# Optimization experiments

Measured on AMD Instinct MI355X. Metric: run time of the kernel, lower is better.

## Reference

```python
import jax, jax.numpy as jnp
import numpy as np

B, S, D = 2, 2048, 1024
H = 16
HD = D // H


def setup_inputs() -> dict:
    key = jax.random.key(0)
    ks = jax.random.split(key, 6)
    X = jax.random.normal(ks[0], (B, S, D), dtype=jnp.float32)
    # Linear weights stored [in, out] so y = x @ W (torch stores transposed).
    sc = 1.0 / np.sqrt(D)
    Wq = jax.random.normal(ks[1], (D, D), dtype=jnp.float32) * sc
    Wk = jax.random.normal(ks[2], (D, D), dtype=jnp.float32) * sc
    Wv = jax.random.normal(ks[3], (D, D), dtype=jnp.float32) * sc
    Wo = jax.random.normal(ks[4], (D, D), dtype=jnp.float32) * sc
    bo = jax.random.normal(ks[5], (D,), dtype=jnp.float32) * 0.01
    return {"X": X, "Wq": Wq, "Wk": Wk, "Wv": Wv, "Wo": Wo, "bo": bo}


def reference(X, Wq, Wk, Wv, Wo, bo):
    b, n, _ = X.shape
    # QKV projections (no bias, qkv_bias=False), reshape to [b, h, n, hd]
    q = (X @ Wq).reshape(b, n, H, HD).transpose(0, 2, 1, 3)
    k = (X @ Wk).reshape(b, n, H, HD).transpose(0, 2, 1, 3)
    v = (X @ Wv).reshape(b, n, H, HD).transpose(0, 2, 1, 3)
    # Unscaled scores (module's scale flag defaults to False)
    scores = jnp.einsum("bhqd,bhkd->bhqk", q, k)
    causal = jnp.triu(jnp.ones((n, n), dtype=bool), k=1)  # True above diagonal
    scores = jnp.where(causal, -jnp.inf, scores)
    attn = jax.nn.softmax(scores, axis=-1)
    # dropout p=0.0 -> identity
    ctx = jnp.einsum("bhqk,bhkd->bqhd", attn, v).reshape(b, n, H * HD)
    return ctx @ Wo + bo
```

## Files before the change

### kernel.cpp

```cpp
#include <hip/hip_runtime.h>
#include <stdint.h>


typedef __attribute__((ext_vector_type(8))) short short8;
typedef __attribute__((ext_vector_type(4))) float floatx4;

#define S_LEN 2048
#define D_DIM 1024
#define NH 16
#define HD 64
#define L2E 1.44269504088896340736f

__device__ __forceinline__ short f2bf(float f) {
    uint32_t u = __builtin_bit_cast(uint32_t, f);
    uint32_t r = u + 0x7fffu + ((u >> 16) & 1u);
    return (short)(r >> 16);
}
__device__ __forceinline__ uint32_t pack2(float a, float b) {
#if __has_builtin(__builtin_amdgcn_cvt_pk_bf16_f32)
    auto v = __builtin_amdgcn_cvt_pk_bf16_f32(a, b);
    uint32_t r; __builtin_memcpy(&r, &v, sizeof(r)); return r;
#else
    return (uint32_t)(uint16_t)f2bf(a) | ((uint32_t)(uint16_t)f2bf(b) << 16);
#endif
}
__device__ __forceinline__ void gll16(const void* g, void* l) {
    __builtin_amdgcn_global_load_lds(
        (const __attribute__((address_space(1))) void*)g,
        (__attribute__((address_space(3))) void*)l, 16, 0, 0);
}

__global__ __launch_bounds__(256) void castx_kernel(const float* __restrict__ X,
                                                    short* __restrict__ Xb) {
    int i = blockIdx.x * 256 + threadIdx.x;
    const float4 v = *(const float4*)(X + (size_t)i * 4);
    uint2 o;
    o.x = pack2(v.x, v.y);
    o.y = pack2(v.z, v.w);
    *(uint2*)(Xb + (size_t)i * 4) = o;
}

__global__ __launch_bounds__(256) void tcast4_kernel(const float* __restrict__ Wq,
                                                     const float* __restrict__ Wk,
                                                     const float* __restrict__ Wv,
                                                     const float* __restrict__ Wo,
                                                     short* __restrict__ WqkvT,
                                                     short* __restrict__ WoT) {
    const int z = blockIdx.z;
    const float* W = (z == 0) ? Wq : (z == 1) ? Wk : (z == 2) ? Wv : Wo;
    short* WT = (z < 3) ? (WqkvT + (size_t)z * 1024 * 1024) : WoT;
    __shared__ float tile[32][33];
    const int bx = blockIdx.x * 32;
    const int by = blockIdx.y * 32;
    const int tx = threadIdx.x, ty = threadIdx.y;
    for (int i = 0; i < 32; i += 8)
        tile[ty + i][tx] = W[(size_t)(bx + ty + i) * D_DIM + by + tx];
    __syncthreads();
    for (int i = 0; i < 32; i += 8)
        WT[(size_t)(by + ty + i) * D_DIM + bx + tx] = f2bf(tile[tx][ty + i]);
}

__device__ __forceinline__ void gemm_main8(const short* __restrict__ A,
                                           const short* __restrict__ BT,
                                           short* As, short* Bs,
                                           int m0, int n0, floatx4 (&acc)[4][2],
                                           int tid) {
    const int lane = tid & 63, ln = lane & 15, quad = lane >> 4;
    const int wave = tid >> 6;
    const int mw = (wave & 1) * 64, nw = (wave >> 1) * 32;
    for (int k0 = 0; k0 < D_DIM; k0 += 64) {
        __syncthreads();
        for (int t = 0; t < 2; t++) {
            const int c = t * 512 + tid;
            const int row = c >> 3, pos = c & 7, src = pos ^ (row & 7);
            gll16(A  + (size_t)(m0 + row) * D_DIM + k0 + src * 8, As + c * 8);
            gll16(BT + (size_t)(n0 + row) * D_DIM + k0 + src * 8, Bs + c * 8);
        }
        __syncthreads();
        for (int ks = 0; ks < 2; ks++) {
            short8 a[4], b[2];
            for (int i = 0; i < 4; i++) {
                const int row = mw + i * 16 + ln;
                a[i] = *(const short8*)(As + row * 64 + (((ks * 4 + quad) ^ (ln & 7)) * 8));
            }
            for (int j = 0; j < 2; j++) {
                const int row = nw + j * 16 + ln;
                b[j] = *(const short8*)(Bs + row * 64 + (((ks * 4 + quad) ^ (ln & 7)) * 8));
            }
            for (int i = 0; i < 4; i++)
                for (int j = 0; j < 2; j++)
                    acc[i][j] = __builtin_amdgcn_mfma_f32_16x16x32_bf16(a[i], b[j], acc[i][j], 0, 0, 0);
        }
    }
}

__global__ __launch_bounds__(512) void gemm_qkv_kernel(const short* __restrict__ Xb,
                                                       const short* __restrict__ WT,
                                                       short* __restrict__ Qb,
                                                       short* __restrict__ Kb,
                                                       short* __restrict__ Vtb) {
    __shared__ __align__(16) short As[128 * 64];
    __shared__ __align__(16) short Bs[128 * 64];
    const int m0 = blockIdx.x * 128, n0 = blockIdx.y * 128;
    floatx4 acc[4][2] = {};
    gemm_main8(Xb, WT, As, Bs, m0, n0, acc, threadIdx.x);

    const int tid = threadIdx.x, wave = tid >> 6, lane = tid & 63;
    const int ln = lane & 15, quad = lane >> 4;
    const int mw = (wave & 1) * 64, nw = (wave >> 1) * 32;
    const int nsel = n0 >> 10;
    const float qs = (nsel == 0) ? L2E : 1.f;
    short* outB = (nsel == 0) ? Qb : (nsel == 1 ? Kb : Vtb);
    for (int i = 0; i < 4; i++)
        for (int j = 0; j < 2; j++)
            for (int r = 0; r < 4; r++) {
                const int row = m0 + mw + i * 16 + quad * 4 + r;
                const int col = (n0 & 1023) + nw + j * 16 + ln;
                const int bb = row >> 11, s = row & (S_LEN - 1);
                const int h = col >> 6, hd = col & (HD - 1);
                const short v = f2bf(acc[i][j][r] * qs);
                if (nsel < 2)
                    outB[(((size_t)(bb * NH + h)) * S_LEN + s) * HD + hd] = v;
                else
                    outB[(((size_t)(bb * NH + h)) * HD + hd) * S_LEN + s] = v;
            }
}

__global__ __launch_bounds__(512) void gemm_out_kernel(const short* __restrict__ Cb,
                                                       const short* __restrict__ WoT,
                                                       float* __restrict__ out,
                                                       const float* __restrict__ bias) {
    __shared__ __align__(16) short As[128 * 64];
    __shared__ __align__(16) short Bs[64 * 64];
    const int m0 = blockIdx.x * 128, n0 = blockIdx.y * 64;
    const int tid = threadIdx.x, lane = tid & 63;
    const int ln = lane & 15, quad = lane >> 4;
    const int wave = tid >> 6;
    const int mw = (wave & 3) * 32, nw = (wave >> 2) * 32;

    floatx4 acc[2][2] = {};

    for (int k0 = 0; k0 < D_DIM; k0 += 64) {
        __syncthreads();
        for (int t = 0; t < 2; t++) {
            const int c = t * 512 + tid;
            const int row = c >> 3, pos = c & 7, src = pos ^ (row & 7);
            gll16(Cb + (size_t)(m0 + row) * D_DIM + k0 + src * 8, As + c * 8);
        }
        {
            const int c = tid;
            const int row = c >> 3, pos = c & 7, src = pos ^ (row & 7);
            gll16(WoT + (size_t)(n0 + row) * D_DIM + k0 + src * 8, Bs + c * 8);
        }
        __syncthreads();
        for (int ks = 0; ks < 2; ks++) {
            short8 a[2], b[2];
            for (int i = 0; i < 2; i++) {
                const int row = mw + i * 16 + ln;
                a[i] = *(const short8*)(As + row * 64 + (((ks * 4 + quad) ^ (ln & 7)) * 8));
            }
            for (int j = 0; j < 2; j++) {
                const int row = nw + j * 16 + ln;
                b[j] = *(const short8*)(Bs + row * 64 + (((ks * 4 + quad) ^ (ln & 7)) * 8));
            }
            for (int i = 0; i < 2; i++)
                for (int j = 0; j < 2; j++)
                    acc[i][j] = __builtin_amdgcn_mfma_f32_16x16x32_bf16(a[i], b[j], acc[i][j], 0, 0, 0);
        }
    }

    for (int i = 0; i < 2; i++)
        for (int j = 0; j < 2; j++)
            for (int r = 0; r < 4; r++) {
                const int row = m0 + mw + i * 16 + quad * 4 + r;
                const int col = n0 + nw + j * 16 + ln;
                out[(size_t)row * D_DIM + col] = acc[i][j][r] + bias[col];
            }
}

#define PST 136

__global__ __launch_bounds__(256, 3) void attn_kernel(const short* __restrict__ Q,
                                                      const short* __restrict__ Kg,
                                                      const short* __restrict__ Vt,
                                                      short* __restrict__ ctx,
                                                      float* __restrict__ Opart,
                                                      float* __restrict__ Lpart) {
    __shared__ __align__(16) short Ks[128 * 64];
    __shared__ __align__(16) short Vs[64 * 128];
    __shared__ __align__(16) short Ps[4][16 * PST];

    const int tid = threadIdx.x, wave = tid >> 6, lane = tid & 63;
    const int ln = lane & 15, quad = lane >> 4;

    const int id = blockIdx.x;
    const int bh = (id & 7) + 8 * ((id >> 3) & 3);
    const int t = id >> 5;
    int qt, k_begin, k_end, pidx;
    if (t < 32) {
        qt = 31 - (t >> 1);
        const int half = t & 1;
        const int n = (qt + 2) >> 1;
        const int h0 = n >> 1;
        k_begin = half ? h0 : 0;
        k_end   = half ? n  : h0;
        pidx = ((qt - 16) * 32 + bh) * 2 + half;
    } else {
        qt = 47 - t;
        k_begin = 0; k_end = (qt + 2) >> 1;
        pidx = -1;
    }
    const int kmask = ((qt + 2) >> 1) - 1;
    const int q0 = qt * 64;
    const int bb = bh >> 4, h = bh & 15;
    short* Pw = &Ps[wave][0];

    const short* qrow = Q + ((size_t)bh * S_LEN + q0 + wave * 16 + ln) * HD;
    const short8 qb0 = *(const short8*)(qrow + quad * 8);
    const short8 qb1 = *(const short8*)(qrow + 32 + quad * 8);
    const int q_abs = q0 + wave * 16 + ln;

    float l_part = 0.f;
    floatx4 o_acc[4] = {};

    for (int kt = k_begin; kt < k_end; kt++) {
        const int k0 = kt * 128;
        __syncthreads();
        for (int tt = 0; tt < 4; tt++) {
            const int c = tt * 256 + tid;
            {
                const int row = c >> 3, pos = c & 7, src = pos ^ (row & 7);
                gll16(Kg + ((size_t)bh * S_LEN + k0 + row) * HD + src * 8, Ks + c * 8);
            }
            {
                const int row = c >> 4, pos = c & 15, src = pos ^ (row & 15);
                gll16(Vt + ((size_t)bh * HD + row) * S_LEN + k0 + src * 8, Vs + c * 8);
            }
        }
        __syncthreads();

        floatx4 sc[8];
        for (int nt = 0; nt < 8; nt++) {
            const int row = nt * 16 + ln;
            const short8 ak0 = *(const short8*)(Ks + row * 64 + ((quad ^ (ln & 7)) * 8));
            const short8 ak1 = *(const short8*)(Ks + row * 64 + (((4 + quad) ^ (ln & 7)) * 8));
            floatx4 z = {};
            z = __builtin_amdgcn_mfma_f32_16x16x32_bf16(ak0, qb0, z, 0, 0, 0);
            z = __builtin_amdgcn_mfma_f32_16x16x32_bf16(ak1, qb1, z, 0, 0, 0);
            sc[nt] = z;
        }

        if (kt == kmask) {
            for (int nt = 0; nt < 8; nt++)
                for (int r = 0; r < 4; r++)
                    if (k0 + nt * 16 + quad * 4 + r > q_abs) sc[nt][r] = -1e30f;
        }

        float ls = 0.f;
        for (int nt = 0; nt < 8; nt++)
            for (int r = 0; r < 4; r++) {
                const float e = exp2f(sc[nt][r]);
                sc[nt][r] = e; ls += e;
            }
        l_part += ls;

        for (int nt = 0; nt < 8; nt++) {
            uint2 u;
            u.x = pack2(sc[nt][0], sc[nt][1]);
            u.y = pack2(sc[nt][2], sc[nt][3]);
            *(uint2*)&Pw[ln * PST + nt * 16 + quad * 4] = u;
        }

        for (int ks = 0; ks < 4; ks++) {
            const short8 bp = *(const short8*)&Pw[ln * PST + ks * 32 + quad * 8];
            for (int dt = 0; dt < 4; dt++) {
                const int row = dt * 16 + ln;
                const short8 av = *(const short8*)(Vs + row * 128 + (((ks * 4 + quad) ^ (ln & 15)) * 8));
                o_acc[dt] = __builtin_amdgcn_mfma_f32_16x16x32_bf16(av, bp, o_acc[dt], 0, 0, 0);
            }
        }
    }

    float l_tot = l_part;
    l_tot += __shfl_xor(l_tot, 16, 64);
    l_tot += __shfl_xor(l_tot, 32, 64);

    if (pidx >= 0) {
        float* Ob = Opart + (size_t)pidx * 4096 + (wave * 16 + ln) * 64;
        for (int dt = 0; dt < 4; dt++)
            *(float4*)(Ob + dt * 16 + quad * 4) = *(float4*)&o_acc[dt];
        if (quad == 0) Lpart[(size_t)pidx * 64 + wave * 16 + ln] = l_tot;
    } else {
        const float rl = 1.f / l_tot;
        for (int dt = 0; dt < 4; dt++) {
            uint2 u;
            u.x = pack2(o_acc[dt][0] * rl, o_acc[dt][1] * rl);
            u.y = pack2(o_acc[dt][2] * rl, o_acc[dt][3] * rl);
            *(uint2*)&Pw[ln * PST + dt * 16 + quad * 4] = u;
        }
        const int qr = lane >> 2, sg = lane & 3;
        for (int c = 0; c < 2; c++) {
            const short8 v = *(const short8*)&Pw[qr * PST + sg * 8 + c * 32];
            const int s = q0 + wave * 16 + qr;
            *(short8*)(ctx + ((size_t)bb * S_LEN + s) * D_DIM + h * HD + sg * 8 + c * 32) = v;
        }
    }
}

__global__ __launch_bounds__(256) void combine_kernel(const float* __restrict__ Opart,
                                                      const float* __restrict__ Lpart,
                                                      short* __restrict__ ctx) {
    const int tile = blockIdx.x;
    const int qt = 16 + (tile >> 5), bh = tile & 31;
    const int bb = bh >> 4, h = bh & 15;
    const int p0 = ((qt - 16) * 32 + bh) * 2;
    const float* O0 = Opart + (size_t)p0 * 4096;
    const float* O1 = O0 + 4096;
    const float* l0 = Lpart + (size_t)p0 * 64;
    const float* l1 = l0 + 64;
    for (int e = threadIdx.x; e < 1024; e += 256) {
        const int q = e >> 4, seg = e & 15;
        const float rl = 1.f / (l0[q] + l1[q]);
        const float4 x0 = *(const float4*)(O0 + q * 64 + seg * 4);
        const float4 x1 = *(const float4*)(O1 + q * 64 + seg * 4);
        uint2 u;
        u.x = pack2((x0.x + x1.x) * rl, (x0.y + x1.y) * rl);
        u.y = pack2((x0.z + x1.z) * rl, (x0.w + x1.w) * rl);
        const int s = qt * 64 + q;
        *(uint2*)(ctx + ((size_t)bb * S_LEN + s) * D_DIM + h * HD + seg * 4) = u;
    }
}

extern "C" void kernel_launch(void* const* d_in, const int* in_sizes, int n_in,
                              void* d_out, int out_size, void* d_ws, size_t ws_size,
                              hipStream_t stream) {
    const float* X  = (const float*)d_in[0];
    const float* Wq = (const float*)d_in[1];
    const float* Wk = (const float*)d_in[2];
    const float* Wv = (const float*)d_in[3];
    const float* Wo = (const float*)d_in[4];
    const float* bo = (const float*)d_in[5];
    float* out = (float*)d_out;

    char* ws = (char*)d_ws;
    const size_t MB = 1024 * 1024;
    short* Xb     = (short*)(ws);
    short* WqkvT  = (short*)(ws + 8  * MB);
    short* Qb     = (short*)(ws + 16 * MB);
    short* Kb     = (short*)(ws + 24 * MB);
    short* Vtb    = (short*)(ws + 32 * MB);
    short* ctxb   = (short*)(ws + 40 * MB);
    short* WoT    = (short*)(ws + 48 * MB);
    float* Opart  = (float*)(ws);
    float* Lpart  = (float*)(ws + 50 * MB);

    castx_kernel<<<4096, 256, 0, stream>>>(X, Xb);
    dim3 tg(32, 32, 4), tb(32, 8);
    tcast4_kernel<<<tg, tb, 0, stream>>>(Wq, Wk, Wv, Wo, WqkvT, WoT);

    dim3 gq(32, 24);
    gemm_qkv_kernel<<<gq, 512, 0, stream>>>(Xb, WqkvT, Qb, Kb, Vtb);

    attn_kernel<<<1536, 256, 0, stream>>>(Qb, Kb, Vtb, ctxb, Opart, Lpart);
    combine_kernel<<<512, 256, 0, stream>>>(Opart, Lpart, ctxb);

    dim3 go(32, 16);
    gemm_out_kernel<<<go, 512, 0, stream>>>(ctxb, WoT, out, bo);
}
```

Measured before the change: 183.6 us.

## Retile attention to 128-query blocks with 64-key tiles and merge prep kernels

The attention kernel now gives each block 128 queries (two 16-row sub-tiles per wave) and streams 64-key K/V tiles. Each K/V tile loaded into shared memory is reused across twice as many queries, and the grid and combine work are rebalanced, with a new split-K schedule for the long causal rows. The X cast and weight transpose-cast kernels are also merged into one launch. In exchange, per-wave register pressure rises, the occupancy hint is dropped, and there are fewer blocks to hide latency and balance the causal triangle.

```diff
diff --git a/kernel.cpp b/kernel.cpp
--- a/kernel.cpp
+++ b/kernel.cpp
@@ -30,34 +30,36 @@
         (__attribute__((address_space(3))) void*)l, 16, 0, 0);
 }
 
-__global__ __launch_bounds__(256) void castx_kernel(const float* __restrict__ X,
-                                                    short* __restrict__ Xb) {
-    int i = blockIdx.x * 256 + threadIdx.x;
-    const float4 v = *(const float4*)(X + (size_t)i * 4);
-    uint2 o;
-    o.x = pack2(v.x, v.y);
-    o.y = pack2(v.z, v.w);
-    *(uint2*)(Xb + (size_t)i * 4) = o;
-}
-
-__global__ __launch_bounds__(256) void tcast4_kernel(const float* __restrict__ Wq,
-                                                     const float* __restrict__ Wk,
-                                                     const float* __restrict__ Wv,
-                                                     const float* __restrict__ Wo,
-                                                     short* __restrict__ WqkvT,
-                                                     short* __restrict__ WoT) {
-    const int z = blockIdx.z;
-    const float* W = (z == 0) ? Wq : (z == 1) ? Wk : (z == 2) ? Wv : Wo;
-    short* WT = (z < 3) ? (WqkvT + (size_t)z * 1024 * 1024) : WoT;
+__global__ __launch_bounds__(256) void prep_kernel(const float* __restrict__ X,
+                                                   const float* __restrict__ Wq,
+                                                   const float* __restrict__ Wk,
+                                                   const float* __restrict__ Wv,
+                                                   const float* __restrict__ Wo,
+                                                   short* __restrict__ Xb,
+                                                   short* __restrict__ WqkvT,
+                                                   short* __restrict__ WoT) {
     __shared__ float tile[32][33];
-    const int bx = blockIdx.x * 32;
-    const int by = blockIdx.y * 32;
-    const int tx = threadIdx.x, ty = threadIdx.y;
-    for (int i = 0; i < 32; i += 8)
-        tile[ty + i][tx] = W[(size_t)(bx + ty + i) * D_DIM + by + tx];
-    __syncthreads();
-    for (int i = 0; i < 32; i += 8)
-        WT[(size_t)(by + ty + i) * D_DIM + bx + tx] = f2bf(tile[tx][ty + i]);
+    const int id = blockIdx.x, tid = threadIdx.x;
+    if (id < 4096) {
+        const int i = id * 256 + tid;
+        const float4 v = *(const float4*)(X + (size_t)i * 4);
+        uint2 o;
+        o.x = pack2(v.x, v.y);
+        o.y = pack2(v.z, v.w);
+        *(uint2*)(Xb + (size_t)i * 4) = o;
+    } else {
+        const int f = id - 4096;
+        const int z = f >> 10, r = f & 1023;
+        const float* W = (z == 0) ? Wq : (z == 1) ? Wk : (z == 2) ? Wv : Wo;
+        short* WT = (z < 3) ? (WqkvT + (size_t)z * 1024 * 1024) : WoT;
+        const int bx = (r & 31) * 32, by = (r >> 5) * 32;
+        const int tx = tid & 31, ty = tid >> 5;
+        for (int i = 0; i < 32; i += 8)
+            tile[ty + i][tx] = W[(size_t)(bx + ty + i) * D_DIM + by + tx];
+        __syncthreads();
+        for (int i = 0; i < 32; i += 8)
+            WT[(size_t)(by + ty + i) * D_DIM + bx + tx] = f2bf(tile[tx][ty + i]);
+    }
 }
 
 __device__ __forceinline__ void gemm_main8(const short* __restrict__ A,
@@ -178,17 +180,17 @@
             }
 }
 
-#define PST 136
-
-__global__ __launch_bounds__(256, 3) void attn_kernel(const short* __restrict__ Q,
-                                                      const short* __restrict__ Kg,
-                                                      const short* __restrict__ Vt,
-                                                      short* __restrict__ ctx,
-                                                      float* __restrict__ Opart,
-                                                      float* __restrict__ Lpart) {
-    __shared__ __align__(16) short Ks[128 * 64];
-    __shared__ __align__(16) short Vs[64 * 128];
-    __shared__ __align__(16) short Ps[4][16 * PST];
+#define PST2 72
+
+__global__ __launch_bounds__(256) void attn_kernel(const short* __restrict__ Q,
+                                                   const short* __restrict__ Kg,
+                                                   const short* __restrict__ Vt,
+                                                   short* __restrict__ ctx,
+                                                   float* __restrict__ Opart,
+                                                   float* __restrict__ Lpart) {
+    __shared__ __align__(16) short Ks[64 * 64];
+    __shared__ __align__(16) short Vs[64 * 64];
+    __shared__ __align__(16) short Ps[4][2 * 16 * PST2];
 
     const int tid = threadIdx.x, wave = tid >> 6, lane = tid & 63;
     const int ln = lane & 15, quad = lane >> 4;
@@ -197,112 +199,126 @@
     const int bh = (id & 7) + 8 * ((id >> 3) & 3);
     const int t = id >> 5;
     int qt, k_begin, k_end, pidx;
-    if (t < 32) {
-        qt = 31 - (t >> 1);
-        const int half = t & 1;
-        const int n = (qt + 2) >> 1;
-        const int h0 = n >> 1;
+    if (t == 0) {
+        qt = 8; k_begin = 0; k_end = 18; pidx = -1;
+    } else if (t <= 14) {
+        qt = 15 - ((t - 1) >> 1);
+        const int half = (t - 1) & 1;
+        const int n = 2 * qt + 2, h0 = n >> 1;
         k_begin = half ? h0 : 0;
         k_end   = half ? n  : h0;
-        pidx = ((qt - 16) * 32 + bh) * 2 + half;
+        pidx = ((qt - 9) * 32 + bh) * 2 + half;
     } else {
-        qt = 47 - t;
-        k_begin = 0; k_end = (qt + 2) >> 1;
+        qt = 22 - t;
+        k_begin = 0; k_end = 2 * qt + 2;
         pidx = -1;
     }
-    const int kmask = ((qt + 2) >> 1) - 1;
-    const int q0 = qt * 64;
+    const int kmask0 = 2 * qt;
+    const int q0 = qt * 128;
     const int bb = bh >> 4, h = bh & 15;
     short* Pw = &Ps[wave][0];
 
-    const short* qrow = Q + ((size_t)bh * S_LEN + q0 + wave * 16 + ln) * HD;
-    const short8 qb0 = *(const short8*)(qrow + quad * 8);
-    const short8 qb1 = *(const short8*)(qrow + 32 + quad * 8);
-    const int q_abs = q0 + wave * 16 + ln;
-
-    float l_part = 0.f;
-    floatx4 o_acc[4] = {};
+    short8 qb[2][2];
+    int q_abs[2];
+    for (int qs = 0; qs < 2; qs++) {
+        const int q = q0 + wave * 32 + qs * 16 + ln;
+        q_abs[qs] = q;
+        const short* qrow = Q + ((size_t)bh * S_LEN + q) * HD;
+        qb[qs][0] = *(const short8*)(qrow + quad * 8);
+        qb[qs][1] = *(const short8*)(qrow + 32 + quad * 8);
+    }
+
+    float l_part[2] = {0.f, 0.f};
+    floatx4 o_acc[2][4] = {};
 
     for (int kt = k_begin; kt < k_end; kt++) {
-        const int k0 = kt * 128;
-        __syncthreads();
-        for (int tt = 0; tt < 4; tt++) {
+        const int k0 = kt * 64;
+        __syncthreads();
+        for (int tt = 0; tt < 2; tt++) {
             const int c = tt * 256 + tid;
-            {
-                const int row = c >> 3, pos = c & 7, src = pos ^ (row & 7);
-                gll16(Kg + ((size_t)bh * S_LEN + k0 + row) * HD + src * 8, Ks + c * 8);
-            }
-            {
-                const int row = c >> 4, pos = c & 15, src = pos ^ (row & 15);
-                gll16(Vt + ((size_t)bh * HD + row) * S_LEN + k0 + src * 8, Vs + c * 8);
-            }
-        }
-        __syncthreads();
-
-        floatx4 sc[8];
-        for (int nt = 0; nt < 8; nt++) {
-            const int row = nt * 16 + ln;
-            const short8 ak0 = *(const short8*)(Ks + row * 64 + ((quad ^ (ln & 7)) * 8));
-            const short8 ak1 = *(const short8*)(Ks + row * 64 + (((4 + quad) ^ (ln & 7)) * 8));
-            floatx4 z = {};
-            z = __builtin_amdgcn_mfma_f32_16x16x32_bf16(ak0, qb0, z, 0, 0, 0);
-            z = __builtin_amdgcn_mfma_f32_16x16x32_bf16(ak1, qb1, z, 0, 0, 0);
-            sc[nt] = z;
-        }
-
-        if (kt == kmask) {
-            for (int nt = 0; nt < 8; nt++)
-                for (int r = 0; r < 4; r++)
-                    if (k0 + nt * 16 + quad * 4 + r > q_abs) sc[nt][r] = -1e30f;
-        }
-
-        float ls = 0.f;
-        for (int nt = 0; nt < 8; nt++)
-            for (int r = 0; r < 4; r++) {
-                const float e = exp2f(sc[nt][r]);
-                sc[nt][r] = e; ls += e;
-            }
-        l_part += ls;
-
-        for (int nt = 0; nt < 8; nt++) {
-            uint2 u;
-            u.x = pack2(sc[nt][0], sc[nt][1]);
-            u.y = pack2(sc[nt][2], sc[nt][3]);
-            *(uint2*)&Pw[ln * PST + nt * 16 + quad * 4] = u;
-        }
-
-        for (int ks = 0; ks < 4; ks++) {
-            const short8 bp = *(const short8*)&Pw[ln * PST + ks * 32 + quad * 8];
+            const int row = c >> 3, pos = c & 7, src = pos ^ (row & 7);
+            gll16(Kg + ((size_t)bh * S_LEN + k0 + row) * HD + src * 8, Ks + c * 8);
+            gll16(Vt + ((size_t)bh * HD + row) * S_LEN + k0 + src * 8, Vs + c * 8);
+        }
+        __syncthreads();
+
+        for (int qs = 0; qs < 2; qs++) {
+            floatx4 sc[4];
+            for (int nt = 0; nt < 4; nt++) {
+                const int row = nt * 16 + ln;
+                const short8 ak0 = *(const short8*)(Ks + row * 64 + ((quad ^ (ln & 7)) * 8));
+                const short8 ak1 = *(const short8*)(Ks + row * 64 + (((4 + quad) ^ (ln & 7)) * 8));
+                floatx4 z = {};
+                z = __builtin_amdgcn_mfma_f32_16x16x32_bf16(ak0, qb[qs][0], z, 0, 0, 0);
+                z = __builtin_amdgcn_mfma_f32_16x16x32_bf16(ak1, qb[qs][1], z, 0, 0, 0);
+                sc[nt] = z;
+            }
+
+            if (kt >= kmask0) {
+                for (int nt = 0; nt < 4; nt++)
+                    for (int r = 0; r < 4; r++)
+                        if (k0 + nt * 16 + quad * 4 + r > q_abs[qs]) sc[nt][r] = -1e30f;
+            }
+
+            float ls = 0.f;
+            for (int nt = 0; nt < 4; nt++)
+                for (int r = 0; r < 4; r++) {
+                    const float e = exp2f(sc[nt][r]);
+                    sc[nt][r] = e; ls += e;
+                }
+            l_part[qs] += ls;
+
+            short* Pq = Pw + qs * 16 * PST2;
+            for (int nt = 0; nt < 4; nt++) {
+                uint2 u;
+                u.x = pack2(sc[nt][0], sc[nt][1]);
+                u.y = pack2(sc[nt][2], sc[nt][3]);
+                *(uint2*)&Pq[ln * PST2 + nt * 16 + quad * 4] = u;
+            }
+
+            for (int ks = 0; ks < 2; ks++) {
+                const short8 bp = *(const short8*)&Pq[ln * PST2 + ks * 32 + quad * 8];
+                for (int dt = 0; dt < 4; dt++) {
+                    const int row = dt * 16 + ln;
+                    const short8 av = *(const short8*)(Vs + row * 64 + (((ks * 4 + quad) ^ (ln & 7)) * 8));
+                    o_acc[qs][dt] = __builtin_amdgcn_mfma_f32_16x16x32_bf16(av, bp, o_acc[qs][dt], 0, 0, 0);
+                }
+            }
+        }
+    }
+
+    float l_tot[2];
+    for (int qs = 0; qs < 2; qs++) {
+        float l = l_part[qs];
+        l += __shfl_xor(l, 16, 64);
+        l += __shfl_xor(l, 32, 64);
+        l_tot[qs] = l;
+    }
+
+    if (pidx >= 0) {
+        for (int qs = 0; qs < 2; qs++) {
+            const int q = wave * 32 + qs * 16 + ln;
+            float* Ob = Opart + (size_t)pidx * 8192 + q * 64;
+            for (int dt = 0; dt < 4; dt++)
+                *(float4*)(Ob + dt * 16 + quad * 4) = *(float4*)&o_acc[qs][dt];
+            if (quad == 0) Lpart[(size_t)pidx * 128 + q] = l_tot[qs];
+        }
+    } else {
+        for (int qs = 0; qs < 2; qs++) {
+            const float rl = 1.f / l_tot[qs];
+            short* Pq = Pw + qs * 16 * PST2;
             for (int dt = 0; dt < 4; dt++) {
-                const int row = dt * 16 + ln;
-                const short8 av = *(const short8*)(Vs + row * 128 + (((ks * 4 + quad) ^ (ln & 15)) * 8));
-                o_acc[dt] = __builtin_amdgcn_mfma_f32_16x16x32_bf16(av, bp, o_acc[dt], 0, 0, 0);
-            }
-        }
-    }
-
-    float l_tot = l_part;
-    l_tot += __shfl_xor(l_tot, 16, 64);
-    l_tot += __shfl_xor(l_tot, 32, 64);
-
-    if (pidx >= 0) {
-        float* Ob = Opart + (size_t)pidx * 4096 + (wave * 16 + ln) * 64;
-        for (int dt = 0; dt < 4; dt++)
-            *(float4*)(Ob + dt * 16 + quad * 4) = *(float4*)&o_acc[dt];
-        if (quad == 0) Lpart[(size_t)pidx * 64 + wave * 16 + ln] = l_tot;
-    } else {
-        const float rl = 1.f / l_tot;
-        for (int dt = 0; dt < 4; dt++) {
-            uint2 u;
-            u.x = pack2(o_acc[dt][0] * rl, o_acc[dt][1] * rl);
-            u.y = pack2(o_acc[dt][2] * rl, o_acc[dt][3] * rl);
-            *(uint2*)&Pw[ln * PST + dt * 16 + quad * 4] = u;
-        }
-        const int qr = lane >> 2, sg = lane & 3;
-        for (int c = 0; c < 2; c++) {
-            const short8 v = *(const short8*)&Pw[qr * PST + sg * 8 + c * 32];
-            const int s = q0 + wave * 16 + qr;
-            *(short8*)(ctx + ((size_t)bb * S_LEN + s) * D_DIM + h * HD + sg * 8 + c * 32) = v;
+                uint2 u;
+                u.x = pack2(o_acc[qs][dt][0] * rl, o_acc[qs][dt][1] * rl);
+                u.y = pack2(o_acc[qs][dt][2] * rl, o_acc[qs][dt][3] * rl);
+                *(uint2*)&Pq[ln * PST2 + dt * 16 + quad * 4] = u;
+            }
+            const int qr = lane >> 2, sg = lane & 3;
+            for (int c = 0; c < 2; c++) {
+                const short8 v = *(const short8*)&Pq[qr * PST2 + sg * 8 + c * 32];
+                const int s = q0 + wave * 32 + qs * 16 + qr;
+                *(short8*)(ctx + ((size_t)bb * S_LEN + s) * D_DIM + h * HD + sg * 8 + c * 32) = v;
+            }
         }
     }
 }
@@ -311,14 +327,14 @@
                                                       const float* __restrict__ Lpart,
                                                       short* __restrict__ ctx) {
     const int tile = blockIdx.x;
-    const int qt = 16 + (tile >> 5), bh = tile & 31;
+    const int qt = 9 + (tile >> 5), bh = tile & 31;
     const int bb = bh >> 4, h = bh & 15;
-    const int p0 = ((qt - 16) * 32 + bh) * 2;
-    const float* O0 = Opart + (size_t)p0 * 4096;
-    const float* O1 = O0 + 4096;
-    const float* l0 = Lpart + (size_t)p0 * 64;
-    const float* l1 = l0 + 64;
-    for (int e = threadIdx.x; e < 1024; e += 256) {
+    const int p0 = ((qt - 9) * 32 + bh) * 2;
+    const float* O0 = Opart + (size_t)p0 * 8192;
+    const float* O1 = O0 + 8192;
+    const float* l0 = Lpart + (size_t)p0 * 128;
+    const float* l1 = l0 + 128;
+    for (int e = threadIdx.x; e < 2048; e += 256) {
         const int q = e >> 4, seg = e & 15;
         const float rl = 1.f / (l0[q] + l1[q]);
         const float4 x0 = *(const float4*)(O0 + q * 64 + seg * 4);
@@ -326,7 +342,7 @@
         uint2 u;
         u.x = pack2((x0.x + x1.x) * rl, (x0.y + x1.y) * rl);
         u.y = pack2((x0.z + x1.z) * rl, (x0.w + x1.w) * rl);
-        const int s = qt * 64 + q;
+        const int s = qt * 128 + q;
         *(uint2*)(ctx + ((size_t)bb * S_LEN + s) * D_DIM + h * HD + seg * 4) = u;
     }
 }
@@ -354,15 +370,13 @@
     float* Opart  = (float*)(ws);
     float* Lpart  = (float*)(ws + 50 * MB);
 
-    castx_kernel<<<4096, 256, 0, stream>>>(X, Xb);
-    dim3 tg(32, 32, 4), tb(32, 8);
-    tcast4_kernel<<<tg, tb, 0, stream>>>(Wq, Wk, Wv, Wo, WqkvT, WoT);
+    prep_kernel<<<8192, 256, 0, stream>>>(X, Wq, Wk, Wv, Wo, Xb, WqkvT, WoT);
 
     dim3 gq(32, 24);
     gemm_qkv_kernel<<<gq, 512, 0, stream>>>(Xb, WqkvT, Qb, Kb, Vtb);
 
-    attn_kernel<<<1536, 256, 0, stream>>>(Qb, Kb, Vtb, ctxb, Opart, Lpart);
-    combine_kernel<<<512, 256, 0, stream>>>(Opart, Lpart, ctxb);
+    attn_kernel<<<736, 256, 0, stream>>>(Qb, Kb, Vtb, ctxb, Opart, Lpart);
+    combine_kernel<<<224, 256, 0, stream>>>(Opart, Lpart, ctxb);
 
     dim3 go(32, 16);
     gemm_out_kernel<<<go, 512, 0, stream>>>(ctxb, WoT, out, bo);
```

New measurement: 204.4 us. 11.4% more time.

## Use 32x32 MFMA in attention with intra-block key split and merge prep kernels

Applied to the files above, without the earlier changes.

The attention kernel moves from 16x16x32 to 32x32x16 bf16 MFMAs. Each wave now owns 32 queries and half of the 128-key tile, and the two key halves are reduced through shared memory at the end, with swizzled P staging replacing the padded layout. Separately, the X cast and the weight transpose-cast kernels are merged into one launch. This aims to cut LDS traffic per MFMA and one kernel launch, at the cost of an extra shared-memory reduction and the loss of the occupancy hint of 3.

```diff
diff --git a/kernel.cpp b/kernel.cpp
--- a/kernel.cpp
+++ b/kernel.cpp
@@ -4,6 +4,7 @@
 
 typedef __attribute__((ext_vector_type(8))) short short8;
 typedef __attribute__((ext_vector_type(4))) float floatx4;
+typedef __attribute__((ext_vector_type(16))) float floatx16;
 
 #define S_LEN 2048
 #define D_DIM 1024
@@ -30,34 +31,36 @@
         (__attribute__((address_space(3))) void*)l, 16, 0, 0);
 }
 
-__global__ __launch_bounds__(256) void castx_kernel(const float* __restrict__ X,
-                                                    short* __restrict__ Xb) {
-    int i = blockIdx.x * 256 + threadIdx.x;
-    const float4 v = *(const float4*)(X + (size_t)i * 4);
-    uint2 o;
-    o.x = pack2(v.x, v.y);
-    o.y = pack2(v.z, v.w);
-    *(uint2*)(Xb + (size_t)i * 4) = o;
-}
-
-__global__ __launch_bounds__(256) void tcast4_kernel(const float* __restrict__ Wq,
-                                                     const float* __restrict__ Wk,
-                                                     const float* __restrict__ Wv,
-                                                     const float* __restrict__ Wo,
-                                                     short* __restrict__ WqkvT,
-                                                     short* __restrict__ WoT) {
-    const int z = blockIdx.z;
-    const float* W = (z == 0) ? Wq : (z == 1) ? Wk : (z == 2) ? Wv : Wo;
-    short* WT = (z < 3) ? (WqkvT + (size_t)z * 1024 * 1024) : WoT;
+__global__ __launch_bounds__(256) void prep_kernel(const float* __restrict__ X,
+                                                   const float* __restrict__ Wq,
+                                                   const float* __restrict__ Wk,
+                                                   const float* __restrict__ Wv,
+                                                   const float* __restrict__ Wo,
+                                                   short* __restrict__ Xb,
+                                                   short* __restrict__ WqkvT,
+                                                   short* __restrict__ WoT) {
     __shared__ float tile[32][33];
-    const int bx = blockIdx.x * 32;
-    const int by = blockIdx.y * 32;
-    const int tx = threadIdx.x, ty = threadIdx.y;
-    for (int i = 0; i < 32; i += 8)
-        tile[ty + i][tx] = W[(size_t)(bx + ty + i) * D_DIM + by + tx];
-    __syncthreads();
-    for (int i = 0; i < 32; i += 8)
-        WT[(size_t)(by + ty + i) * D_DIM + bx + tx] = f2bf(tile[tx][ty + i]);
+    const int id = blockIdx.x, tid = threadIdx.x;
+    if (id < 4096) {
+        const int i = id * 256 + tid;
+        const float4 v = *(const float4*)(X + (size_t)i * 4);
+        uint2 o;
+        o.x = pack2(v.x, v.y);
+        o.y = pack2(v.z, v.w);
+        *(uint2*)(Xb + (size_t)i * 4) = o;
+    } else {
+        const int f = id - 4096;
+        const int z = f >> 10, r = f & 1023;
+        const float* W = (z == 0) ? Wq : (z == 1) ? Wk : (z == 2) ? Wv : Wo;
+        short* WT = (z < 3) ? (WqkvT + (size_t)z * 1024 * 1024) : WoT;
+        const int bx = (r & 31) * 32, by = (r >> 5) * 32;
+        const int tx = tid & 31, ty = tid >> 5;
+        for (int i = 0; i < 32; i += 8)
+            tile[ty + i][tx] = W[(size_t)(bx + ty + i) * D_DIM + by + tx];
+        __syncthreads();
+        for (int i = 0; i < 32; i += 8)
+            WT[(size_t)(by + ty + i) * D_DIM + bx + tx] = f2bf(tile[tx][ty + i]);
+    }
 }
 
 __device__ __forceinline__ void gemm_main8(const short* __restrict__ A,
@@ -178,20 +181,22 @@
             }
 }
 
-#define PST 136
-
-__global__ __launch_bounds__(256, 3) void attn_kernel(const short* __restrict__ Q,
-                                                      const short* __restrict__ Kg,
-                                                      const short* __restrict__ Vt,
-                                                      short* __restrict__ ctx,
-                                                      float* __restrict__ Opart,
-                                                      float* __restrict__ Lpart) {
-    __shared__ __align__(16) short Ks[128 * 64];
-    __shared__ __align__(16) short Vs[64 * 128];
-    __shared__ __align__(16) short Ps[4][16 * PST];
+__global__ __launch_bounds__(256) void attn_kernel(const short* __restrict__ Q,
+                                                   const short* __restrict__ Kg,
+                                                   const short* __restrict__ Vt,
+                                                   short* __restrict__ ctx,
+                                                   float* __restrict__ Opart,
+                                                   float* __restrict__ Lpart) {
+    __shared__ __align__(16) short SMEM[24704];
+    short* Ks = SMEM;
+    short* Vs = SMEM + 8192;
+    short* Ps = SMEM + 16384;
+    float* Lpool = (float*)(SMEM + 24576);
+    float* Opool = (float*)SMEM;
 
     const int tid = threadIdx.x, wave = tid >> 6, lane = tid & 63;
-    const int ln = lane & 15, quad = lane >> 4;
+    const int lq = lane & 31, lh = lane >> 5;
+    const int qsel = wave & 1, ksel = wave >> 1;
 
     const int id = blockIdx.x;
     const int bh = (id & 7) + 8 * ((id >> 3) & 3);
@@ -213,15 +218,17 @@
     const int kmask = ((qt + 2) >> 1) - 1;
     const int q0 = qt * 64;
     const int bb = bh >> 4, h = bh & 15;
-    short* Pw = &Ps[wave][0];
-
-    const short* qrow = Q + ((size_t)bh * S_LEN + q0 + wave * 16 + ln) * HD;
-    const short8 qb0 = *(const short8*)(qrow + quad * 8);
-    const short8 qb1 = *(const short8*)(qrow + 32 + quad * 8);
-    const int q_abs = q0 + wave * 16 + ln;
+    const int kbase = ksel * 64;
+    short* Pq = Ps + wave * 2048;
+
+    const int q_abs = q0 + qsel * 32 + lq;
+    const short* qrow = Q + ((size_t)bh * S_LEN + q_abs) * HD;
+    short8 qb[4];
+    for (int tt = 0; tt < 4; tt++)
+        qb[tt] = *(const short8*)(qrow + tt * 16 + lh * 8);
 
     float l_part = 0.f;
-    floatx4 o_acc[4] = {};
+    floatx16 o_acc[2] = {};
 
     for (int kt = k_begin; kt < k_end; kt++) {
         const int k0 = kt * 128;
@@ -239,70 +246,107 @@
         }
         __syncthreads();
 
-        floatx4 sc[8];
-        for (int nt = 0; nt < 8; nt++) {
-            const int row = nt * 16 + ln;
-            const short8 ak0 = *(const short8*)(Ks + row * 64 + ((quad ^ (ln & 7)) * 8));
-            const short8 ak1 = *(const short8*)(Ks + row * 64 + (((4 + quad) ^ (ln & 7)) * 8));
-            floatx4 z = {};
-            z = __builtin_amdgcn_mfma_f32_16x16x32_bf16(ak0, qb0, z, 0, 0, 0);
-            z = __builtin_amdgcn_mfma_f32_16x16x32_bf16(ak1, qb1, z, 0, 0, 0);
-            sc[nt] = z;
+        floatx16 sc[2];
+        for (int m = 0; m < 2; m++) {
+            const int row = kbase + m * 32 + lq;
+            floatx16 z = {};
+            for (int tt = 0; tt < 4; tt++) {
+                const short8 ak = *(const short8*)(Ks + row * 64 + (((tt * 2 + lh) ^ (lq & 7)) * 8));
+                z = __builtin_amdgcn_mfma_f32_32x32x16_bf16(ak, qb[tt], z, 0, 0, 0);
+            }
+            sc[m] = z;
         }
 
         if (kt == kmask) {
-            for (int nt = 0; nt < 8; nt++)
-                for (int r = 0; r < 4; r++)
-                    if (k0 + nt * 16 + quad * 4 + r > q_abs) sc[nt][r] = -1e30f;
+            for (int m = 0; m < 2; m++)
+                for (int reg = 0; reg < 16; reg++) {
+                    const int kglob = k0 + kbase + m * 32 + (reg & 3) + 8 * (reg >> 2) + 4 * lh;
+                    if (kglob > q_abs) sc[m][reg] = -1e30f;
+                }
         }
 
         float ls = 0.f;
-        for (int nt = 0; nt < 8; nt++)
-            for (int r = 0; r < 4; r++) {
-                const float e = exp2f(sc[nt][r]);
-                sc[nt][r] = e; ls += e;
+        for (int m = 0; m < 2; m++)
+            for (int reg = 0; reg < 16; reg++) {
+                const float e = exp2f(sc[m][reg]);
+                sc[m][reg] = e; ls += e;
             }
         l_part += ls;
 
-        for (int nt = 0; nt < 8; nt++) {
-            uint2 u;
-            u.x = pack2(sc[nt][0], sc[nt][1]);
-            u.y = pack2(sc[nt][2], sc[nt][3]);
-            *(uint2*)&Pw[ln * PST + nt * 16 + quad * 4] = u;
-        }
-
-        for (int ks = 0; ks < 4; ks++) {
-            const short8 bp = *(const short8*)&Pw[ln * PST + ks * 32 + quad * 8];
-            for (int dt = 0; dt < 4; dt++) {
-                const int row = dt * 16 + ln;
-                const short8 av = *(const short8*)(Vs + row * 128 + (((ks * 4 + quad) ^ (ln & 15)) * 8));
-                o_acc[dt] = __builtin_amdgcn_mfma_f32_16x16x32_bf16(av, bp, o_acc[dt], 0, 0, 0);
-            }
-        }
-    }
-
-    float l_tot = l_part;
-    l_tot += __shfl_xor(l_tot, 16, 64);
-    l_tot += __shfl_xor(l_tot, 32, 64);
-
-    if (pidx >= 0) {
-        float* Ob = Opart + (size_t)pidx * 4096 + (wave * 16 + ln) * 64;
-        for (int dt = 0; dt < 4; dt++)
-            *(float4*)(Ob + dt * 16 + quad * 4) = *(float4*)&o_acc[dt];
-        if (quad == 0) Lpart[(size_t)pidx * 64 + wave * 16 + ln] = l_tot;
-    } else {
-        const float rl = 1.f / l_tot;
-        for (int dt = 0; dt < 4; dt++) {
-            uint2 u;
-            u.x = pack2(o_acc[dt][0] * rl, o_acc[dt][1] * rl);
-            u.y = pack2(o_acc[dt][2] * rl, o_acc[dt][3] * rl);
-            *(uint2*)&Pw[ln * PST + dt * 16 + quad * 4] = u;
-        }
-        const int qr = lane >> 2, sg = lane & 3;
-        for (int c = 0; c < 2; c++) {
-            const short8 v = *(const short8*)&Pw[qr * PST + sg * 8 + c * 32];
-            const int s = q0 + wave * 16 + qr;
-            *(short8*)(ctx + ((size_t)bb * S_LEN + s) * D_DIM + h * HD + sg * 8 + c * 32) = v;
+        for (int m = 0; m < 2; m++)
+            for (int rg = 0; rg < 4; rg++) {
+                uint2 u;
+                u.x = pack2(sc[m][rg * 4 + 0], sc[m][rg * 4 + 1]);
+                u.y = pack2(sc[m][rg * 4 + 2], sc[m][rg * 4 + 3]);
+                *(uint2*)&Pq[lq * 64 + (((m * 4 + rg) ^ (lq & 7)) * 8) + 4 * lh] = u;
+            }
+        short8 bp[4];
+        for (int g = 0; g < 4; g++)
+            bp[g] = *(const short8*)&Pq[lq * 64 + (((g * 2 + lh) ^ (lq & 7)) * 8)];
+
+        for (int dt = 0; dt < 2; dt++) {
+            const int row = dt * 32 + lq;
+            for (int g = 0; g < 4; g++) {
+                const int seg = (kbase >> 3) + g * 2 + lh;
+                const short8 av = *(const short8*)(Vs + row * 128 + ((seg ^ (lq & 15)) * 8));
+                o_acc[dt] = __builtin_amdgcn_mfma_f32_32x32x16_bf16(av, bp[g], o_acc[dt], 0, 0, 0);
+            }
+        }
+    }
+
+    l_part += __shfl_xor(l_part, 32, 64);
+
+    __syncthreads();
+    if (ksel == 1) {
+        float* Op = Opool + qsel * 32 * 68;
+        for (int dt = 0; dt < 2; dt++)
+            for (int rg = 0; rg < 4; rg++) {
+                float4 v;
+                v.x = o_acc[dt][rg * 4 + 0]; v.y = o_acc[dt][rg * 4 + 1];
+                v.z = o_acc[dt][rg * 4 + 2]; v.w = o_acc[dt][rg * 4 + 3];
+                *(float4*)&Op[lq * 68 + dt * 32 + 8 * rg + 4 * lh] = v;
+            }
+        if (lane < 32) Lpool[qsel * 32 + lq] = l_part;
+    }
+    __syncthreads();
+    if (ksel == 0) {
+        const float* Op = Opool + qsel * 32 * 68;
+        float om[2][16];
+        for (int dt = 0; dt < 2; dt++)
+            for (int rg = 0; rg < 4; rg++) {
+                const float4 v = *(const float4*)&Op[lq * 68 + dt * 32 + 8 * rg + 4 * lh];
+                om[dt][rg * 4 + 0] = o_acc[dt][rg * 4 + 0] + v.x;
+                om[dt][rg * 4 + 1] = o_acc[dt][rg * 4 + 1] + v.y;
+                om[dt][rg * 4 + 2] = o_acc[dt][rg * 4 + 2] + v.z;
+                om[dt][rg * 4 + 3] = o_acc[dt][rg * 4 + 3] + v.w;
+            }
+        const float l_tot = l_part + Lpool[qsel * 32 + lq];
+
+        if (pidx >= 0) {
+            float* Ob = Opart + (size_t)pidx * 4096 + (qsel * 32 + lq) * 64;
+            for (int dt = 0; dt < 2; dt++)
+                for (int rg = 0; rg < 4; rg++) {
+                    float4 v;
+                    v.x = om[dt][rg * 4 + 0]; v.y = om[dt][rg * 4 + 1];
+                    v.z = om[dt][rg * 4 + 2]; v.w = om[dt][rg * 4 + 3];
+                    *(float4*)(Ob + dt * 32 + 8 * rg + 4 * lh) = v;
+                }
+            if (lane < 32) Lpart[(size_t)pidx * 64 + qsel * 32 + lq] = l_tot;
+        } else {
+            const float rl = 1.f / l_tot;
+            for (int dt = 0; dt < 2; dt++)
+                for (int rg = 0; rg < 4; rg++) {
+                    uint2 u;
+                    u.x = pack2(om[dt][rg * 4 + 0] * rl, om[dt][rg * 4 + 1] * rl);
+                    u.y = pack2(om[dt][rg * 4 + 2] * rl, om[dt][rg * 4 + 3] * rl);
+                    *(uint2*)&Pq[lq * 64 + (((dt * 4 + rg) ^ (lq & 7)) * 8) + 4 * lh] = u;
+                }
+            const int qr = lane >> 1, sg = lane & 1;
+            for (int c = 0; c < 4; c++) {
+                const short8 v = *(const short8*)&Pq[qr * 64 + (((c * 2 + sg) ^ (qr & 7)) * 8)];
+                const int s = q0 + qsel * 32 + qr;
+                *(short8*)(ctx + ((size_t)bb * S_LEN + s) * D_DIM + h * HD + c * 16 + sg * 8) = v;
+            }
         }
     }
 }
@@ -354,9 +398,7 @@
     float* Opart  = (float*)(ws);
     float* Lpart  = (float*)(ws + 50 * MB);
 
-    castx_kernel<<<4096, 256, 0, stream>>>(X, Xb);
-    dim3 tg(32, 32, 4), tb(32, 8);
-    tcast4_kernel<<<tg, tb, 0, stream>>>(Wq, Wk, Wv, Wo, WqkvT, WoT);
+    prep_kernel<<<8192, 256, 0, stream>>>(X, Wq, Wk, Wv, Wo, Xb, WqkvT, WoT);
 
     dim3 gq(32, 24);
     gemm_qkv_kernel<<<gq, 512, 0, stream>>>(Xb, WqkvT, Qb, Kb, Vtb);
```

Result: no change. 186.3 us (+1.5%).
